# Performance work log

Measured on AMD Instinct MI355X. Metric: run time of the kernel, lower is better.

## Reference

```python
import jax, jax.numpy as jnp
import numpy as np

MARGIN = 0.0
BINS = 10
ALPHA = 0.75
N = 16777216  # 2**24 pairs


def setup_inputs() -> dict:
    key = jax.random.key(0)
    k1, k2, k3 = jax.random.split(key, 3)
    output1 = jax.random.normal(k1, (N,), dtype=jnp.float32)
    output2 = jax.random.normal(k2, (N,), dtype=jnp.float32)
    target = jax.random.randint(k3, (N,), 0, 2, dtype=jnp.int64)
    return {"output1": output1, "output2": output2, "target": target}


def reference(output1, output2, target):
    dtype = output1.dtype
    t = target.astype(dtype)
    diff = output1 - output2
    # MarginRankingLoss(reduction='none'): max(0, -target*(x1-x2) + margin)
    loss = jnp.maximum(0.0, -t * diff + MARGIN)
    # gradient-norm proxy g in (0,1)
    expected_sign = 2.0 * t - 1.0
    g = jax.nn.sigmoid(-diff * expected_sign + MARGIN)
    g_norm = jnp.abs(g)
    edges = jnp.arange(BINS + 1, dtype=dtype) / BINS
    # histogram over BINS bins (fixed small loop over bins, vectorized over N)
    counts = jnp.stack([
        jnp.sum((g_norm >= edges[i]) & (g_norm < edges[i + 1]))
        for i in range(BINS)
    ]).astype(dtype)
    tot = jnp.clip(counts, 1.0)
    w = tot ** (-ALPHA)  # per-bin weight; constant wrt g in the original (.item() detaches)
    w = jax.lax.stop_gradient(w)
    bin_idx = jnp.clip(jnp.floor(g * BINS).astype(jnp.int32), 0, BINS - 1)
    sample_weights = w[bin_idx]
    return jnp.mean(loss * sample_weights)
```

## Files before the change

kernel.cpp:

```cpp
#include <hip/hip_runtime.h>

#define BINS 10
#define ALPHA 0.75f

constexpr int NB    = 2048;
constexpr int NT    = 256;
constexpr int ITERS = 8;
constexpr int NT2   = 1024;

__device__ __constant__ float LTH[9] = {
    2.19722458f,  1.38629436f,  0.847297861f, 0.405465108f, 0.0f,
   -0.405465108f, -0.847297861f, -1.38629436f, -2.19722458f};

#define GHM_PROC(AX, BX, TX) do {                                    \
    float diff = (AX) - (BX);                                        \
    float nd   = -diff;                                              \
    bool  tt   = (TX) != 0;                                          \
    float u    = tt ? diff : nd;                                     \
    float loss = tt ? fmaxf(nd, 0.0f) : 0.0f;                        \
    cls[0] += loss;                                                  \
    _Pragma("unroll")                                                \
    for (int k = 1; k < BINS; ++k) {                                 \
      bool p = (u <= LTH[k - 1]);                                    \
      cls[k] += p ? loss : 0.0f;                                     \
      cnt[k] += (unsigned int)p;                                     \
    }                                                                \
  } while (0)

#define GHM_PROC4(AV, BV, TV) do {                                   \
    GHM_PROC((AV).x, (BV).x, (TV).x);                                \
    GHM_PROC((AV).y, (BV).y, (TV).y);                                \
    GHM_PROC((AV).z, (BV).z, (TV).z);                                \
    GHM_PROC((AV).w, (BV).w, (TV).w);                                \
  } while (0)

__global__ __launch_bounds__(NT) void ghm_pass1(
    const float* __restrict__ o1f, const float* __restrict__ o2f,
    const int* __restrict__ tgt, float* __restrict__ lsum_part,
    unsigned int* __restrict__ cnt_part, int n)
{
  const float4* o1 = reinterpret_cast<const float4*>(o1f);
  const float4* o2 = reinterpret_cast<const float4*>(o2f);
  const int4*   tg = reinterpret_cast<const int4*>(tgt);

  float        cls[BINS];
  unsigned int cnt[BINS];
#pragma unroll
  for (int b = 0; b < BINS; ++b) { cls[b] = 0.0f; cnt[b] = 0u; }

  if (n == NB * NT * ITERS * 4 && gridDim.x == NB) {
    const int base = blockIdx.x * (NT * ITERS) + threadIdx.x;
    float4 a0 = o1[base];      float4 b0 = o2[base];      int4 t0 = tg[base];
    float4 a1 = o1[base + NT]; float4 b1 = o2[base + NT]; int4 t1 = tg[base + NT];
#pragma unroll
    for (int k = 0; k < ITERS - 2; ++k) {
      float4 a2 = o1[base + (k + 2) * NT];
      float4 b2 = o2[base + (k + 2) * NT];
      int4   t2 = tg[base + (k + 2) * NT];
      __builtin_amdgcn_sched_barrier(0);
      GHM_PROC4(a0, b0, t0);
      a0 = a1; b0 = b1; t0 = t1;
      a1 = a2; b1 = b2; t1 = t2;
    }
    GHM_PROC4(a0, b0, t0);
    GHM_PROC4(a1, b1, t1);
  } else {
    const int tid = blockIdx.x * NT + threadIdx.x;
    const int stride = gridDim.x * NT;
    const int n4 = n >> 2;
    for (int i = tid; i < n4; i += stride) {
      float4 a  = o1[i];
      float4 bb = o2[i];
      int4   t  = tg[i];
      GHM_PROC4(a, bb, t);
    }
    if (tid == 0) {
      for (int i = n4 * 4; i < n; ++i) GHM_PROC(o1f[i], o2f[i], tgt[i]);
    }
  }

  const int lane = threadIdx.x & 63;
  const int wv   = threadIdx.x >> 6;
  __shared__ float        s_ls[NT / 64][BINS];
  __shared__ unsigned int s_c [NT / 64][BINS];
#pragma unroll
  for (int b = 0; b < BINS; ++b) {
    float v = cls[b];
    unsigned int cv = cnt[b];
#pragma unroll
    for (int off = 32; off >= 1; off >>= 1) {
      v  += __shfl_down(v, off, 64);
      cv += __shfl_down(cv, off, 64);
    }
    if (lane == 0) { s_ls[wv][b] = v; s_c[wv][b] = cv; }
  }
  __syncthreads();
  if (threadIdx.x < BINS) {
    float v = 0.0f; unsigned int cv = 0u;
#pragma unroll
    for (int w = 0; w < NT / 64; ++w) { v += s_ls[w][threadIdx.x]; cv += s_c[w][threadIdx.x]; }
    lsum_part[threadIdx.x * gridDim.x + blockIdx.x] = v;
    cnt_part [threadIdx.x * gridDim.x + blockIdx.x] = cv;
  }
}

__global__ __launch_bounds__(NT2) void ghm_pass2(
    const float* __restrict__ lsum_part, const unsigned int* __restrict__ cnt_part,
    float* __restrict__ out, int nparts, int n)
{
  double             cls[BINS];
  unsigned long long cc [BINS];
#pragma unroll
  for (int b = 0; b < BINS; ++b) { cls[b] = 0.0; cc[b] = 0ull; }

  for (int i = threadIdx.x; i < nparts; i += NT2) {
#pragma unroll
    for (int b = 0; b < BINS; ++b) {
      cls[b] += (double)lsum_part[b * nparts + i];
      cc[b]  += (unsigned long long)cnt_part[b * nparts + i];
    }
  }

  const int lane = threadIdx.x & 63;
  const int wv   = threadIdx.x >> 6;
  __shared__ double             s_ls[NT2 / 64][BINS];
  __shared__ unsigned long long s_c [NT2 / 64][BINS];
#pragma unroll
  for (int b = 0; b < BINS; ++b) {
    double v = cls[b];
    unsigned long long cv = cc[b];
#pragma unroll
    for (int off = 32; off >= 1; off >>= 1) {
      v  += __shfl_down(v, off, 64);
      cv += __shfl_down(cv, off, 64);
    }
    if (lane == 0) { s_ls[wv][b] = v; s_c[wv][b] = cv; }
  }
  __syncthreads();
  if (threadIdx.x == 0) {
    double             CLS[BINS + 1];
    unsigned long long CC [BINS + 1];
#pragma unroll
    for (int b = 0; b < BINS; ++b) {
      double lv = 0.0; unsigned long long cv = 0ull;
#pragma unroll
      for (int w = 0; w < NT2 / 64; ++w) { lv += s_ls[w][b]; cv += s_c[w][b]; }
      CLS[b] = lv; CC[b] = cv;
    }
    CLS[BINS] = 0.0; CC[BINS] = 0ull;
    CC[0] = (unsigned long long)n;

    double total = 0.0;
#pragma unroll
    for (int b = 0; b < BINS; ++b) {
      double lsb            = CLS[b] - CLS[b + 1];
      unsigned long long cb = CC[b] - CC[b + 1];
      float cf  = (float)cb;
      float tot = fmaxf(cf, 1.0f);
      float wgt = powf(tot, -ALPHA);
      total += lsb * (double)wgt;
    }
    out[0] = (float)(total / (double)n);
  }
}

extern "C" void kernel_launch(void* const* d_in, const int* in_sizes, int n_in,
                              void* d_out, int out_size, void* d_ws, size_t ws_size,
                              hipStream_t stream) {
  const float* o1  = (const float*)d_in[0];
  const float* o2  = (const float*)d_in[1];
  const int*   tgt = (const int*)d_in[2];
  float* out = (float*)d_out;
  const int n = in_sizes[0];

  int nb = NB;
  size_t need = (size_t)nb * BINS * (sizeof(float) + sizeof(unsigned int));
  while (nb > 1 && need > ws_size) { nb >>= 1; need >>= 1; }
  float* lsum_part = (float*)d_ws;
  unsigned int* cnt_part = (unsigned int*)((char*)d_ws + (size_t)nb * BINS * sizeof(float));

  ghm_pass1<<<nb, NT, 0, stream>>>(o1, o2, tgt, lsum_part, cnt_part, n);
  ghm_pass2<<<1, NT2, 0, stream>>>(lsum_part, cnt_part, out, nb, n);
}
```

Baseline: 220.7 us.

## Stage inputs via global_load_lds triple buffer and reduce partials with atomics

Input tiles are no longer prefetched into registers. They now go through direct global-to-LDS async loads into a three-deep shared-memory ring, with explicit vmcnt waits. The aim is to hide memory latency without using as many registers. The second pass, which reduced per-block partials, is replaced by double and uint atomics into a tiny workspace plus a trivial finalize kernel, and the workspace is zeroed with a memset. This adds atomic contention on 10 addresses from 2048 blocks, an extra memset launch, and order-dependent floating-point sums.

```diff
diff --git a/kernel.cpp b/kernel.cpp
--- a/kernel.cpp
+++ b/kernel.cpp
@@ -5,10 +5,10 @@
 
 constexpr int NB    = 2048;
 constexpr int NT    = 256;
+constexpr int NWV   = NT / 64;
 constexpr int ITERS = 8;
-constexpr int NT2   = 1024;
 
-__device__ __constant__ float LTH[9] = {
+__device__ constexpr float LTH[9] = {
     2.19722458f,  1.38629436f,  0.847297861f, 0.405465108f, 0.0f,
    -0.405465108f, -0.847297861f, -1.38629436f, -2.19722458f};
 
@@ -34,10 +34,16 @@
     GHM_PROC((AV).w, (BV).w, (TV).w);                                \
   } while (0)
 
+__device__ __forceinline__ void gl_lds16(const void* g, void* l) {
+  __builtin_amdgcn_global_load_lds(
+      (const __attribute__((address_space(1))) unsigned int*)g,
+      (__attribute__((address_space(3))) unsigned int*)l, 16, 0, 0);
+}
+
 __global__ __launch_bounds__(NT) void ghm_pass1(
     const float* __restrict__ o1f, const float* __restrict__ o2f,
-    const int* __restrict__ tgt, float* __restrict__ lsum_part,
-    unsigned int* __restrict__ cnt_part, int n)
+    const int* __restrict__ tgt, double* __restrict__ gls,
+    unsigned int* __restrict__ gcnt, int n)
 {
   const float4* o1 = reinterpret_cast<const float4*>(o1f);
   const float4* o2 = reinterpret_cast<const float4*>(o2f);
@@ -48,22 +54,38 @@
 #pragma unroll
   for (int b = 0; b < BINS; ++b) { cls[b] = 0.0f; cnt[b] = 0u; }
 
+  const int lane = threadIdx.x & 63;
+  const int wv   = threadIdx.x >> 6;
+
+  __shared__ float4 La[3][NWV][64];
+  __shared__ float4 Lb[3][NWV][64];
+  __shared__ int4   Lt[3][NWV][64];
+
   if (n == NB * NT * ITERS * 4 && gridDim.x == NB) {
-    const int base = blockIdx.x * (NT * ITERS) + threadIdx.x;
-    float4 a0 = o1[base];      float4 b0 = o2[base];      int4 t0 = tg[base];
-    float4 a1 = o1[base + NT]; float4 b1 = o2[base + NT]; int4 t1 = tg[base + NT];
+    const int gbase = blockIdx.x * (NT * ITERS);
+
+#define STAGE(K, BUF) do {                                            \
+      const int gi = gbase + (K) * NT + (int)threadIdx.x;             \
+      gl_lds16(&o1[gi], &La[BUF][wv][0]);                             \
+      gl_lds16(&o2[gi], &Lb[BUF][wv][0]);                             \
+      gl_lds16(&tg[gi], &Lt[BUF][wv][0]);                             \
+    } while (0)
+
+    STAGE(0, 0);
+    STAGE(1, 1);
+
 #pragma unroll
-    for (int k = 0; k < ITERS - 2; ++k) {
-      float4 a2 = o1[base + (k + 2) * NT];
-      float4 b2 = o2[base + (k + 2) * NT];
-      int4   t2 = tg[base + (k + 2) * NT];
-      __builtin_amdgcn_sched_barrier(0);
-      GHM_PROC4(a0, b0, t0);
-      a0 = a1; b0 = b1; t0 = t1;
-      a1 = a2; b1 = b2; t1 = t2;
+    for (int k = 0; k < ITERS; ++k) {
+      if (k == ITERS - 1) asm volatile("s_waitcnt vmcnt(0)" ::: "memory");
+      else                asm volatile("s_waitcnt vmcnt(3)" ::: "memory");
+      const int buf = k % 3;
+      float4 a = La[buf][wv][lane];
+      float4 b = Lb[buf][wv][lane];
+      int4   t = Lt[buf][wv][lane];
+      if (k + 2 < ITERS) { STAGE(k + 2, (k + 2) % 3); }
+      GHM_PROC4(a, b, t);
     }
-    GHM_PROC4(a0, b0, t0);
-    GHM_PROC4(a1, b1, t1);
+#undef STAGE
   } else {
     const int tid = blockIdx.x * NT + threadIdx.x;
     const int stride = gridDim.x * NT;
@@ -79,10 +101,8 @@
     }
   }
 
-  const int lane = threadIdx.x & 63;
-  const int wv   = threadIdx.x >> 6;
-  __shared__ float        s_ls[NT / 64][BINS];
-  __shared__ unsigned int s_c [NT / 64][BINS];
+  __shared__ float        s_ls[NWV][BINS];
+  __shared__ unsigned int s_c [NWV][BINS];
 #pragma unroll
   for (int b = 0; b < BINS; ++b) {
     float v = cls[b];
@@ -98,55 +118,21 @@
   if (threadIdx.x < BINS) {
     float v = 0.0f; unsigned int cv = 0u;
 #pragma unroll
-    for (int w = 0; w < NT / 64; ++w) { v += s_ls[w][threadIdx.x]; cv += s_c[w][threadIdx.x]; }
-    lsum_part[threadIdx.x * gridDim.x + blockIdx.x] = v;
-    cnt_part [threadIdx.x * gridDim.x + blockIdx.x] = cv;
+    for (int w = 0; w < NWV; ++w) { v += s_ls[w][threadIdx.x]; cv += s_c[w][threadIdx.x]; }
+    atomicAdd(&gls[threadIdx.x], (double)v);
+    if (cv) atomicAdd(&gcnt[threadIdx.x], cv);
   }
 }
 
-__global__ __launch_bounds__(NT2) void ghm_pass2(
-    const float* __restrict__ lsum_part, const unsigned int* __restrict__ cnt_part,
-    float* __restrict__ out, int nparts, int n)
+__global__ void ghm_final(const double* __restrict__ gls,
+                          const unsigned int* __restrict__ gcnt,
+                          float* __restrict__ out, int n)
 {
-  double             cls[BINS];
-  unsigned long long cc [BINS];
-#pragma unroll
-  for (int b = 0; b < BINS; ++b) { cls[b] = 0.0; cc[b] = 0ull; }
-
-  for (int i = threadIdx.x; i < nparts; i += NT2) {
-#pragma unroll
-    for (int b = 0; b < BINS; ++b) {
-      cls[b] += (double)lsum_part[b * nparts + i];
-      cc[b]  += (unsigned long long)cnt_part[b * nparts + i];
-    }
-  }
-
-  const int lane = threadIdx.x & 63;
-  const int wv   = threadIdx.x >> 6;
-  __shared__ double             s_ls[NT2 / 64][BINS];
-  __shared__ unsigned long long s_c [NT2 / 64][BINS];
-#pragma unroll
-  for (int b = 0; b < BINS; ++b) {
-    double v = cls[b];
-    unsigned long long cv = cc[b];
-#pragma unroll
-    for (int off = 32; off >= 1; off >>= 1) {
-      v  += __shfl_down(v, off, 64);
-      cv += __shfl_down(cv, off, 64);
-    }
-    if (lane == 0) { s_ls[wv][b] = v; s_c[wv][b] = cv; }
-  }
-  __syncthreads();
   if (threadIdx.x == 0) {
     double             CLS[BINS + 1];
     unsigned long long CC [BINS + 1];
 #pragma unroll
-    for (int b = 0; b < BINS; ++b) {
-      double lv = 0.0; unsigned long long cv = 0ull;
-#pragma unroll
-      for (int w = 0; w < NT2 / 64; ++w) { lv += s_ls[w][b]; cv += s_c[w][b]; }
-      CLS[b] = lv; CC[b] = cv;
-    }
+    for (int b = 0; b < BINS; ++b) { CLS[b] = gls[b]; CC[b] = gcnt[b]; }
     CLS[BINS] = 0.0; CC[BINS] = 0ull;
     CC[0] = (unsigned long long)n;
 
@@ -173,12 +159,10 @@
   float* out = (float*)d_out;
   const int n = in_sizes[0];
 
-  int nb = NB;
-  size_t need = (size_t)nb * BINS * (sizeof(float) + sizeof(unsigned int));
-  while (nb > 1 && need > ws_size) { nb >>= 1; need >>= 1; }
-  float* lsum_part = (float*)d_ws;
-  unsigned int* cnt_part = (unsigned int*)((char*)d_ws + (size_t)nb * BINS * sizeof(float));
+  double*       gls  = (double*)d_ws;
+  unsigned int* gcnt = (unsigned int*)((char*)d_ws + BINS * sizeof(double));
+  hipMemsetAsync(d_ws, 0, BINS * (sizeof(double) + sizeof(unsigned int)), stream);
 
-  ghm_pass1<<<nb, NT, 0, stream>>>(o1, o2, tgt, lsum_part, cnt_part, n);
-  ghm_pass2<<<1, NT2, 0, stream>>>(lsum_part, cnt_part, out, nb, n);
+  ghm_pass1<<<NB, NT, 0, stream>>>(o1, o2, tgt, gls, gcnt, n);
+  ghm_final<<<1, 64, 0, stream>>>(gls, gcnt, out, n);
 }
```

After: 218.7 us. No clear change (-0.9%).
